# Kernel tuning notes

Measured on AMD Instinct MI355X. Metric: run time of the kernel, lower is better.

## Reference

```python
import jax, jax.numpy as jnp
import numpy as np

HEAD_DIM = 64
FEAT_DIM = 64
WINDOW = 64
EPS = 1e-6


def _performer_phi(x, proj):
    # x: [..., D] float32, proj: [F, D]  ->  [..., F]
    scaled = x / (HEAD_DIM ** 0.25)
    projected = jnp.einsum('...d,fd->...f', scaled, proj)
    sq_norm = 0.5 * jnp.sum(scaled * scaled, axis=-1, keepdims=True)
    logits = jnp.clip(projected - sq_norm, -20.0, 20.0)
    return jnp.exp(logits) / np.sqrt(float(FEAT_DIM))


def setup_inputs() -> dict:
    key = jax.random.key(0)
    kq, kk, kv, kp = jax.random.split(key, 4)
    B, H, Hkv, T, D = 2, 32, 8, 4096, HEAD_DIM
    q = jax.random.normal(kq, (B, H, T, D), dtype=jnp.float32)
    k = jax.random.normal(kk, (B, Hkv, T, D), dtype=jnp.float32)
    v = jax.random.normal(kv, (B, Hkv, T, D), dtype=jnp.float32)
    # performer projection: orthogonal block, row-normalized (as in _build_projection_matrix)
    g = np.asarray(jax.random.normal(kp, (D, D), dtype=jnp.float32))
    qm, _ = np.linalg.qr(g)
    mat = qm[:, :FEAT_DIM].T  # [F, D]
    mat = mat / np.maximum(np.linalg.norm(mat, axis=-1, keepdims=True), 1e-6)
    proj = jnp.asarray(mat, dtype=jnp.float32)
    return {'q': q, 'k': k, 'v': v, 'proj': proj}


def reference(q, k, v, proj):
    # Hybrid attention: exact local-window softmax (current + previous block,
    # causal) fused with linear (Performer) attention over all fully-evicted
    # blocks via a recurrent SSD state, sharing a single normalizer.
    B, H, T, D = q.shape
    Hkv = k.shape[1]
    G = H // Hkv  # query heads per kv group (query_to_kv = arange(H) // G)
    W = WINDOW
    nb = T // W
    f32 = jnp.float32

    phi_q = _performer_phi(q.astype(f32), proj.astype(f32))  # [B,H,T,F]
    phi_k = _performer_phi(k.astype(f32), proj.astype(f32))  # [B,Hkv,T,F]

    pq = phi_q.reshape(B, Hkv, G, nb, W, FEAT_DIM)
    pk = phi_k.reshape(B, Hkv, nb, W, FEAT_DIM)
    qb = q.astype(f32).reshape(B, Hkv, G, nb, W, D)
    kb = k.astype(f32).reshape(B, Hkv, nb, W, D)
    vb = v.astype(f32).reshape(B, Hkv, nb, W, D)

    # ---- linear-attention recurrent state (state_decay = 1.0 -> plain cumsum)
    # state at query block c covers all blocks <= c-2 (blocks fully outside the
    # local window).
    S_blk = jnp.einsum('bknwf,bknwd->bknfd', pk, vb)  # [B,Hkv,nb,F,D]
    z_blk = pk.sum(axis=3)                            # [B,Hkv,nb,F]
    S_cum = jnp.cumsum(S_blk, axis=2)
    z_cum = jnp.cumsum(z_blk, axis=2)
    S_used = jnp.concatenate([jnp.zeros_like(S_cum[:, :, :2]), S_cum[:, :, :-2]], axis=2)
    z_used = jnp.concatenate([jnp.zeros_like(z_cum[:, :, :2]), z_cum[:, :, :-2]], axis=2)

    num_lin = jnp.einsum('bkgnwf,bknfd->bkgnwd', pq, S_used)  # [B,Hkv,G,nb,W,D]
    den_lin = jnp.einsum('bkgnwf,bknf->bkgnw', pq, z_used)    # [B,Hkv,G,nb,W]

    # ---- local softmax attention over [previous block | current block]
    k_prev = jnp.concatenate([jnp.zeros_like(kb[:, :, :1]), kb[:, :, :-1]], axis=2)
    v_prev = jnp.concatenate([jnp.zeros_like(vb[:, :, :1]), vb[:, :, :-1]], axis=2)
    kk2 = jnp.concatenate([k_prev, kb], axis=3)  # [B,Hkv,nb,2W,D]
    vv2 = jnp.concatenate([v_prev, vb], axis=3)

    scores = jnp.einsum('bkgnwd,bknxd->bkgnwx', qb, kk2) / np.sqrt(float(D))
    jj = jnp.arange(W)[:, None]        # query offset in block
    ii = jnp.arange(2 * W)[None, :]    # key offset in 2-block window
    causal = ii <= (W + jj)            # [W, 2W]
    has_prev = (jnp.arange(nb) > 0)[:, None, None]
    mask = causal[None] & (has_prev | (ii >= W)[None])  # [nb, W, 2W]
    a = jnp.where(mask[None, None, None], jnp.exp(jnp.clip(scores, -30.0, 30.0)), 0.0)

    num_loc = jnp.einsum('bkgnwx,bknxd->bkgnwd', a, vv2)
    den = a.sum(axis=-1) + den_lin + EPS  # shared normalizer

    out = (num_loc + num_lin) / den[..., None]
    return out.reshape(B, H, T, D).astype(q.dtype)
```

## Files before the change

### kernel.cpp

```cpp
#include <hip/hip_runtime.h>

#define BB 2
#define HKV 8
#define HH 32
#define TT 4096
#define NBLK 64
#define SCL 0.35355339059327373f
#define LOG2E 1.4426950408889634f

typedef __attribute__((ext_vector_type(8))) short short8;
typedef __attribute__((ext_vector_type(4))) float f32x4;
typedef unsigned int u32;

__device__ __forceinline__ unsigned short f2bf(float x) {
    union { float f; u32 u; } v; v.f = x;
    u32 r = v.u + 0x7fffu + ((v.u >> 16) & 1u);
    return (unsigned short)(r >> 16);
}
__device__ __forceinline__ u32 pk2(float lo, float hi) {
    u32 r;
    asm("v_cvt_pk_bf16_f32 %0, %1, %2" : "=v"(r) : "v"(lo), "v"(hi));
    return r;
}
__device__ __forceinline__ float bf2f(unsigned short b) {
    union { u32 u; float f; } v; v.u = ((u32)b) << 16; return v.f;
}
__device__ __forceinline__ f32x4 mfma16(short8 a, short8 b, f32x4 c) {
    return __builtin_amdgcn_mfma_f32_16x16x32_bf16(a, b, c, 0, 0, 0);
}
__device__ __forceinline__ short8 ldsfrag(const char* base, int row, int off) {
    int b = (row << 7) + off;
    b ^= (row & 7) << 4;
    return *(const short8*)(base + b);
}
__device__ __forceinline__ short8 xform(f32x4 t0, f32x4 t1, int lane) {
    const int c = lane & 15, g = lane >> 4;
    u32 p00 = pk2(t0[0], t0[1]), p01 = pk2(t0[2], t0[3]);
    u32 p10 = pk2(t1[0], t1[1]), p11 = pk2(t1[2], t1[3]);
    int srcA = c + 32 * (g & 1);
    int srcB = srcA + 16;
    u32 a00 = (u32)__shfl((int)p00, srcA);
    u32 a01 = (u32)__shfl((int)p01, srcA);
    u32 a10 = (u32)__shfl((int)p10, srcA);
    u32 a11 = (u32)__shfl((int)p11, srcA);
    u32 b00 = (u32)__shfl((int)p00, srcB);
    u32 b01 = (u32)__shfl((int)p01, srcB);
    u32 b10 = (u32)__shfl((int)p10, srcB);
    u32 b11 = (u32)__shfl((int)p11, srcB);
    bool hi = (g & 2);
    union { u32 u[4]; short8 s; } r;
    r.u[0] = hi ? a10 : a00;
    r.u[1] = hi ? a11 : a01;
    r.u[2] = hi ? b10 : b00;
    r.u[3] = hi ? b11 : b01;
    return r.s;
}
__device__ __forceinline__ void gld16(const void* g, void* l) {
    __builtin_amdgcn_global_load_lds((const __attribute__((address_space(1))) u32*)g,
                                     (__attribute__((address_space(3))) u32*)l, 16, 0, 0);
}

__global__ __launch_bounds__(256, 4) void k_phase1(
        const float* __restrict__ kg, const float* __restrict__ vg,
        const float* __restrict__ pg,
        char* __restrict__ sblk, char* __restrict__ kbf, char* __restrict__ vbf,
        float* __restrict__ zg) {
    __shared__ __align__(16) char kb_s[8192];
    __shared__ __align__(16) char vt_s[8192];
    __shared__ float sqn_s[64];

    const int tid = threadIdx.x;
    const int bid = blockIdx.x;
    const size_t base = (size_t)bid * 4096;

#pragma unroll
    for (int j = 0; j < 4; ++j) {
        int i4 = tid + j * 256;
        int key = i4 >> 4, d0 = (i4 & 15) << 2;
        float4 fk = *(const float4*)(kg + base + key * 64 + d0);
        float s0 = fk.x * SCL, s1 = fk.y * SCL, s2 = fk.z * SCL, s3 = fk.w * SCL;
        int byte = (key << 7) + (d0 << 1); byte ^= (key & 7) << 4;
        *(uint2*)(kb_s + byte) = make_uint2(pk2(s0, s1), pk2(s2, s3));
        float ps = 0.5f * (s0 * s0 + s1 * s1 + s2 * s2 + s3 * s3);
        ps += __shfl_xor(ps, 1);
        ps += __shfl_xor(ps, 2);
        ps += __shfl_xor(ps, 4);
        ps += __shfl_xor(ps, 8);
        if ((tid & 15) == 0) sqn_s[key] = ps;
    }
    {
        int d = tid & 63, kq = tid >> 6;
        const float* vp = vg + base + (size_t)kq * 16 * 64 + d;
        union { unsigned short h[16]; uint4 q[2]; } pk;
#pragma unroll
        for (int i = 0; i < 16; ++i) pk.h[i] = f2bf(vp[i * 64]);
        int b0 = ((d << 7) + (kq << 5)) ^ ((d & 7) << 4);
        int b1 = ((d << 7) + (kq << 5) + 16) ^ ((d & 7) << 4);
        *(uint4*)(vt_s + b0) = pk.q[0];
        *(uint4*)(vt_s + b1) = pk.q[1];
    }
    __syncthreads();

    {
        int off = tid * 16;
        *(float4*)(kbf + (size_t)bid * 8192 + off) = *(const float4*)(kb_s + off);
        *(float4*)(kbf + (size_t)bid * 8192 + off + 4096) = *(const float4*)(kb_s + off + 4096);
        *(float4*)(vbf + (size_t)bid * 8192 + off) = *(const float4*)(vt_s + off);
        *(float4*)(vbf + (size_t)bid * 8192 + off + 4096) = *(const float4*)(vt_s + off + 4096);
    }

    const int lane = tid & 63, wv = tid >> 6;
    const int c = lane & 15, g = lane >> 4;
    const int fb = wv * 16;

    const float* prow = pg + (size_t)(fb + c) * 64;
    short8 pjb[2];
#pragma unroll
    for (int kt = 0; kt < 2; ++kt) {
        int d0 = kt * 32 + g * 8;
        float4 f0 = *(const float4*)(prow + d0);
        float4 f1 = *(const float4*)(prow + d0 + 4);
        union { u32 u[4]; short8 s; } r;
        r.u[0] = pk2(f0.x, f0.y); r.u[1] = pk2(f0.z, f0.w);
        r.u[2] = pk2(f1.x, f1.y); r.u[3] = pk2(f1.z, f1.w);
        pjb[kt] = r.s;
    }

    f32x4 pc[4];
    float zp = 0.f;
#pragma unroll
    for (int t = 0; t < 4; ++t) {
        f32x4 s = {0.f, 0.f, 0.f, 0.f};
        s = mfma16(ldsfrag(kb_s, t * 16 + c, g * 16), pjb[0], s);
        s = mfma16(ldsfrag(kb_s, t * 16 + c, g * 16 + 64), pjb[1], s);
#pragma unroll
        for (int r = 0; r < 4; ++r) {
            int w = t * 16 + g * 4 + r;
            float p = exp2f(fmaf(s[r] - sqn_s[w], LOG2E, -3.0f));
            s[r] = p;
            zp += p;
        }
        pc[t] = s;
    }
    zp += __shfl_xor(zp, 16);
    zp += __shfl_xor(zp, 32);
    if (lane < 16) zg[(size_t)bid * 64 + fb + c] = zp;

    short8 pb0 = xform(pc[0], pc[1], lane);
    short8 pb1 = xform(pc[2], pc[3], lane);

    char* so = sblk + (size_t)bid * 8192;
#pragma unroll
    for (int dt = 0; dt < 4; ++dt) {
        f32x4 s = {0.f, 0.f, 0.f, 0.f};
        s = mfma16(ldsfrag(vt_s, dt * 16 + c, g * 16), pb0, s);
        s = mfma16(ldsfrag(vt_s, dt * 16 + c, g * 16 + 64), pb1, s);
#pragma unroll
        for (int r = 0; r < 4; ++r) {
            int d = dt * 16 + g * 4 + r;
            int byte = ((d << 7) + ((fb + c) << 1)) ^ ((d & 7) << 4);
            *(unsigned short*)(so + byte) = f2bf(s[r]);
        }
    }
}

__global__ __launch_bounds__(256) void k_scan(char* __restrict__ sblk,
                                              float* __restrict__ zg,
                                              const float* __restrict__ pg,
                                              char* __restrict__ pbf) {
    const int tid = threadIdx.x;
    const int bx = blockIdx.x;
    if (bx < 128) {
        int pair = bx >> 3;
        int u = ((bx & 7) << 8) + tid;
        char* p = sblk + (size_t)pair * 64 * 8192 + (size_t)u * 4;
        float c0a = 0.f, c1a = 0.f, c0b = 0.f, c1b = 0.f;
        for (int n = 0; n < 64; ++n) {
            u32 w = *(const u32*)(p + (size_t)n * 8192);
            float va = bf2f((unsigned short)(w & 0xffff));
            float vb = bf2f((unsigned short)(w >> 16));
            *(u32*)(p + (size_t)n * 8192) = pk2(c0a, c0b);
            c0a = c1a; c1a += va;
            c0b = c1b; c1b += vb;
        }
    } else if (bx < 132) {
        int i = ((bx - 128) << 8) + tid;
        int pair = i >> 6, f = i & 63;
        float* zp = zg + (size_t)pair * 64 * 64 + f;
        float c0 = 0.f, c1 = 0.f;
        for (int n = 0; n < 64; ++n) {
            float val = zp[(size_t)n * 64];
            zp[(size_t)n * 64] = c0;
            c0 = c1; c1 += val;
        }
    } else {
#pragma unroll
        for (int j = 0; j < 4; ++j) {
            int i4 = tid + j * 256;
            int row = i4 >> 4, d0 = (i4 & 15) << 2;
            float4 f = *(const float4*)(pg + row * 64 + d0);
            int byte = ((row << 7) + (d0 << 1)) ^ ((row & 7) << 4);
            *(uint2*)(pbf + byte) = make_uint2(pk2(f.x, f.y), pk2(f.z, f.w));
        }
    }
}

__global__ __launch_bounds__(256, 4) void k_main(
        const float* __restrict__ qg,
        const char* __restrict__ kbf, const char* __restrict__ vbf,
        const char* __restrict__ sbf, const char* __restrict__ pbf,
        const float* __restrict__ zg, float* __restrict__ outg) {
    __shared__ __align__(16) char smem[24576];

    const int tid = threadIdx.x;
    const int orig = blockIdx.x;
    const int bid = (orig & 7) * 512 + (orig >> 3);
    const int n = bid & 63;
    const int h = (bid >> 6) & 31;
    const int b = bid >> 11;
    const int kv = h >> 2;
    const int iblk = ((b * HKV + kv) << 6) + n;
    const int lane = tid & 63, wv = tid >> 6;
    const int c = lane & 15, g = lane >> 4;
    const bool hasprev = (n > 0);

    const size_t qrow0 = (size_t)(b * HH + h) * TT + (size_t)n * 64;
    const int qr = wv * 16 + c;
    const float* qrow = qg + (qrow0 + qr) * 64;
    float4 qf[4];
    qf[0] = *(const float4*)(qrow + g * 8);
    qf[1] = *(const float4*)(qrow + g * 8 + 4);
    qf[2] = *(const float4*)(qrow + 32 + g * 8);
    qf[3] = *(const float4*)(qrow + 32 + g * 8 + 4);

    {
        const char* gs[3] = {kbf + (size_t)(iblk - 1) * 8192, kbf + (size_t)iblk * 8192,
                             vbf + (size_t)iblk * 8192};
#pragma unroll
        for (int ci = 0; ci < 6; ++ci) {
            int cch = wv * 6 + ci;
            int seg = cch >> 3, off = (cch & 7) << 10;
            if (n == 0 && seg == 0) continue;
            gld16(gs[seg] + off + lane * 16, smem + (seg << 13) + off);
        }
        if (n == 0) {
            uint4 zz = {0, 0, 0, 0};
            *(uint4*)(smem + tid * 32) = zz;
            *(uint4*)(smem + tid * 32 + 16) = zz;
        }
    }

    float4 zv[4];
#pragma unroll
    for (int ft = 0; ft < 4; ++ft)
        zv[ft] = *(const float4*)(zg + (size_t)iblk * 64 + ft * 16 + g * 4);

    float sq = 0.f;
    short8 qb[2];
#pragma unroll
    for (int kt = 0; kt < 2; ++kt) {
        float4 f0 = qf[kt * 2], f1 = qf[kt * 2 + 1];
        float s0 = f0.x * SCL, s1 = f0.y * SCL, s2 = f0.z * SCL, s3 = f0.w * SCL;
        float s4 = f1.x * SCL, s5 = f1.y * SCL, s6 = f1.z * SCL, s7 = f1.w * SCL;
        sq += s0 * s0 + s1 * s1 + s2 * s2 + s3 * s3 + s4 * s4 + s5 * s5 + s6 * s6 + s7 * s7;
        union { u32 u[4]; short8 s; } r;
        r.u[0] = pk2(s0, s1); r.u[1] = pk2(s2, s3);
        r.u[2] = pk2(s4, s5); r.u[3] = pk2(s6, s7);
        qb[kt] = r.s;
    }
    sq += __shfl_xor(sq, 16);
    sq += __shfl_xor(sq, 32);
    const float sqn = 0.5f * sq;

    __syncthreads();

    const char* K2 = smem;
    const char* VTP = smem;
    const char* VTC = smem + 16384;
    const char* PJ = pbf;

    short8 ab[4];
    float asum = 0.f;
#pragma unroll
    for (int p = 0; p < 4; ++p) {
        if (p == 2) {
            __syncthreads();
            if (hasprev) {
                const char* vp = vbf + (size_t)(iblk - 1) * 8192;
                gld16(vp + ((wv * 2 + 0) << 10) + lane * 16, smem + ((wv * 2 + 0) << 10));
                gld16(vp + ((wv * 2 + 1) << 10) + lane * 16, smem + ((wv * 2 + 1) << 10));
            }
        }
        f32x4 t0, t1;
#pragma unroll
        for (int half = 0; half < 2; ++half) {
            int t = p * 2 + half;
            f32x4 sc = {0.f, 0.f, 0.f, 0.f};
            sc = mfma16(ldsfrag(K2, t * 16 + c, g * 16), qb[0], sc);
            sc = mfma16(ldsfrag(K2, t * 16 + c, g * 16 + 64), qb[1], sc);
#pragma unroll
            for (int r = 0; r < 4; ++r) {
                int key = t * 16 + g * 4 + r;
                bool valid = (key >= 64) ? ((key - 64) <= qr) : hasprev;
                float a = valid ? __expf(sc[r]) : 0.f;
                sc[r] = a;
                asum += a;
            }
            if (half == 0) t0 = sc; else t1 = sc;
        }
        ab[p] = xform(t0, t1, lane);
    }
    asum += __shfl_xor(asum, 16);
    asum += __shfl_xor(asum, 32);

    float dl = 0.f;
    short8 pb[2];
#pragma unroll
    for (int pp = 0; pp < 2; ++pp) {
        f32x4 u0, u1;
#pragma unroll
        for (int half = 0; half < 2; ++half) {
            int ft = pp * 2 + half;
            f32x4 pf = {0.f, 0.f, 0.f, 0.f};
            pf = mfma16(ldsfrag(PJ, ft * 16 + c, g * 16), qb[0], pf);
            pf = mfma16(ldsfrag(PJ, ft * 16 + c, g * 16 + 64), qb[1], pf);
#pragma unroll
            for (int r = 0; r < 4; ++r) {
                float pv = exp2f(fmaf(pf[r] - sqn, LOG2E, -3.0f));
                pf[r] = pv;
                dl += pv * ((const float*)&zv[ft])[r];
            }
            if (half == 0) u0 = pf; else u1 = pf;
        }
        pb[pp] = xform(u0, u1, lane);
    }
    dl += __shfl_xor(dl, 16);
    dl += __shfl_xor(dl, 32);

    __syncthreads();

    const char* stp = sbf + (size_t)iblk * 8192;
    const float inv = 1.f / (asum + dl + 1e-6f);
    float* orow = outg + (qrow0 + qr) * 64;
#pragma unroll
    for (int dt = 0; dt < 4; ++dt) {
        f32x4 a4 = {0.f, 0.f, 0.f, 0.f};
        a4 = mfma16(ldsfrag(VTP, dt * 16 + c, g * 16), ab[0], a4);
        a4 = mfma16(ldsfrag(VTP, dt * 16 + c, g * 16 + 64), ab[1], a4);
        a4 = mfma16(ldsfrag(VTC, dt * 16 + c, g * 16), ab[2], a4);
        a4 = mfma16(ldsfrag(VTC, dt * 16 + c, g * 16 + 64), ab[3], a4);
        a4 = mfma16(ldsfrag(stp, dt * 16 + c, g * 16), pb[0], a4);
        a4 = mfma16(ldsfrag(stp, dt * 16 + c, g * 16 + 64), pb[1], a4);
#pragma unroll
        for (int r = 0; r < 4; ++r)
            orow[dt * 16 + g * 4 + r] = a4[r] * inv;
    }
}

extern "C" void kernel_launch(void* const* d_in, const int* in_sizes, int n_in,
                              void* d_out, int out_size, void* d_ws, size_t ws_size,
                              hipStream_t stream) {
    const float* q = (const float*)d_in[0];
    const float* k = (const float*)d_in[1];
    const float* v = (const float*)d_in[2];
    const float* proj = (const float*)d_in[3];
    float* out = (float*)d_out;

    char* ws = (char*)d_ws;
    char* sblk = ws;
    char* kbf = ws + (8u << 20);
    char* vbf = ws + (16u << 20);
    float* z = (float*)(ws + (24u << 20));
    char* pbf = ws + (24u << 20) + (256u << 10);

    k_phase1<<<dim3(1024), dim3(256), 0, stream>>>(k, v, proj, sblk, kbf, vbf, z);
    k_scan<<<dim3(133), dim3(256), 0, stream>>>(sblk, z, proj, pbf);
    k_main<<<dim3(4096), dim3(256), 0, stream>>>(q, kbf, vbf, sblk, pbf, z, out);
}
```

Measured before the change: 59.91 us.

## Process strips of four blocks per workgroup with triple-buffered K/V prefetch

```diff
diff --git a/kernel.cpp b/kernel.cpp
--- a/kernel.cpp
+++ b/kernel.cpp
@@ -5,6 +5,7 @@
 #define HH 32
 #define TT 4096
 #define NBLK 64
+#define STRIP 4
 #define SCL 0.35355339059327373f
 #define LOG2E 1.4426950408889634f
 
@@ -175,23 +176,34 @@
         int u = ((bx & 7) << 8) + tid;
         char* p = sblk + (size_t)pair * 64 * 8192 + (size_t)u * 4;
         float c0a = 0.f, c1a = 0.f, c0b = 0.f, c1b = 0.f;
-        for (int n = 0; n < 64; ++n) {
-            u32 w = *(const u32*)(p + (size_t)n * 8192);
-            float va = bf2f((unsigned short)(w & 0xffff));
-            float vb = bf2f((unsigned short)(w >> 16));
-            *(u32*)(p + (size_t)n * 8192) = pk2(c0a, c0b);
-            c0a = c1a; c1a += va;
-            c0b = c1b; c1b += vb;
+        for (int n8 = 0; n8 < 64; n8 += 8) {
+            u32 w[8];
+#pragma unroll
+            for (int j = 0; j < 8; ++j)
+                w[j] = *(const u32*)(p + (size_t)(n8 + j) * 8192);
+#pragma unroll
+            for (int j = 0; j < 8; ++j) {
+                *(u32*)(p + (size_t)(n8 + j) * 8192) = pk2(c0a, c0b);
+                float va = bf2f((unsigned short)(w[j] & 0xffff));
+                float vb = bf2f((unsigned short)(w[j] >> 16));
+                c0a = c1a; c1a += va;
+                c0b = c1b; c1b += vb;
+            }
         }
     } else if (bx < 132) {
         int i = ((bx - 128) << 8) + tid;
         int pair = i >> 6, f = i & 63;
         float* zp = zg + (size_t)pair * 64 * 64 + f;
         float c0 = 0.f, c1 = 0.f;
-        for (int n = 0; n < 64; ++n) {
-            float val = zp[(size_t)n * 64];
-            zp[(size_t)n * 64] = c0;
-            c0 = c1; c1 += val;
+        for (int n8 = 0; n8 < 64; n8 += 8) {
+            float w[8];
+#pragma unroll
+            for (int j = 0; j < 8; ++j) w[j] = zp[(size_t)(n8 + j) * 64];
+#pragma unroll
+            for (int j = 0; j < 8; ++j) {
+                zp[(size_t)(n8 + j) * 64] = c0;
+                c0 = c1; c1 += w[j];
+            }
         }
     } else {
 #pragma unroll
@@ -205,155 +217,194 @@
     }
 }
 
-__global__ __launch_bounds__(256, 4) void k_main(
+__global__ __launch_bounds__(256, 3) void k_main(
         const float* __restrict__ qg,
         const char* __restrict__ kbf, const char* __restrict__ vbf,
         const char* __restrict__ sbf, const char* __restrict__ pbf,
         const float* __restrict__ zg, float* __restrict__ outg) {
-    __shared__ __align__(16) char smem[24576];
+    __shared__ __align__(16) char smem[49152];
 
     const int tid = threadIdx.x;
     const int orig = blockIdx.x;
-    const int bid = (orig & 7) * 512 + (orig >> 3);
-    const int n = bid & 63;
-    const int h = (bid >> 6) & 31;
-    const int b = bid >> 11;
-    const int kv = h >> 2;
-    const int iblk = ((b * HKV + kv) << 6) + n;
+    const int bid = (orig & 7) * 128 + (orig >> 3);
+    const int gq = bid & 3;
+    const int strip = (bid >> 2) & 15;
+    const int kv = (bid >> 6) & 7;
+    const int b = (bid >> 9) & 1;
+    const int h = kv * 4 + gq;
+    const int n0 = strip * STRIP;
+    const int iblk0 = ((b * HKV + kv) << 6) + n0;
     const int lane = tid & 63, wv = tid >> 6;
     const int c = lane & 15, g = lane >> 4;
-    const bool hasprev = (n > 0);
-
-    const size_t qrow0 = (size_t)(b * HH + h) * TT + (size_t)n * 64;
     const int qr = wv * 16 + c;
-    const float* qrow = qg + (qrow0 + qr) * 64;
+
+    {
+        const char* gs[4] = {kbf + (size_t)(iblk0 - 1) * 8192, kbf + (size_t)iblk0 * 8192,
+                             vbf + (size_t)(iblk0 - 1) * 8192, vbf + (size_t)iblk0 * 8192};
+        const int ls[4] = {0, 8192, 24576, 32768};
+#pragma unroll
+        for (int ci = 0; ci < 8; ++ci) {
+            int cch = wv * 8 + ci;
+            int seg = cch >> 3, off = (cch & 7) << 10;
+            if (n0 == 0 && (seg == 0 || seg == 2)) continue;
+            gld16(gs[seg] + off + lane * 16, smem + ls[seg] + off);
+        }
+        if (n0 == 0) {
+            uint4 zz = {0, 0, 0, 0};
+            *(uint4*)(smem + 24576 + tid * 32) = zz;
+            *(uint4*)(smem + 24576 + tid * 32 + 16) = zz;
+        }
+    }
+
+    short8 pja[8];
+#pragma unroll
+    for (int ft = 0; ft < 4; ++ft) {
+        pja[ft * 2 + 0] = ldsfrag(pbf, ft * 16 + c, g * 16);
+        pja[ft * 2 + 1] = ldsfrag(pbf, ft * 16 + c, g * 16 + 64);
+    }
+
+    const size_t qhead = (size_t)(b * HH + h) * TT;
     float4 qf[4];
-    qf[0] = *(const float4*)(qrow + g * 8);
-    qf[1] = *(const float4*)(qrow + g * 8 + 4);
-    qf[2] = *(const float4*)(qrow + 32 + g * 8);
-    qf[3] = *(const float4*)(qrow + 32 + g * 8 + 4);
-
     {
-        const char* gs[3] = {kbf + (size_t)(iblk - 1) * 8192, kbf + (size_t)iblk * 8192,
-                             vbf + (size_t)iblk * 8192};
-#pragma unroll
-        for (int ci = 0; ci < 6; ++ci) {
-            int cch = wv * 6 + ci;
-            int seg = cch >> 3, off = (cch & 7) << 10;
-            if (n == 0 && seg == 0) continue;
-            gld16(gs[seg] + off + lane * 16, smem + (seg << 13) + off);
-        }
-        if (n == 0) {
-            uint4 zz = {0, 0, 0, 0};
-            *(uint4*)(smem + tid * 32) = zz;
-            *(uint4*)(smem + tid * 32 + 16) = zz;
-        }
-    }
-
+        const float* qrow = qg + (qhead + (size_t)n0 * 64 + qr) * 64;
+        qf[0] = *(const float4*)(qrow + g * 8);
+        qf[1] = *(const float4*)(qrow + g * 8 + 4);
+        qf[2] = *(const float4*)(qrow + 32 + g * 8);
+        qf[3] = *(const float4*)(qrow + 32 + g * 8 + 4);
+    }
     float4 zv[4];
 #pragma unroll
     for (int ft = 0; ft < 4; ++ft)
-        zv[ft] = *(const float4*)(zg + (size_t)iblk * 64 + ft * 16 + g * 4);
-
-    float sq = 0.f;
-    short8 qb[2];
-#pragma unroll
-    for (int kt = 0; kt < 2; ++kt) {
-        float4 f0 = qf[kt * 2], f1 = qf[kt * 2 + 1];
-        float s0 = f0.x * SCL, s1 = f0.y * SCL, s2 = f0.z * SCL, s3 = f0.w * SCL;
-        float s4 = f1.x * SCL, s5 = f1.y * SCL, s6 = f1.z * SCL, s7 = f1.w * SCL;
-        sq += s0 * s0 + s1 * s1 + s2 * s2 + s3 * s3 + s4 * s4 + s5 * s5 + s6 * s6 + s7 * s7;
-        union { u32 u[4]; short8 s; } r;
-        r.u[0] = pk2(s0, s1); r.u[1] = pk2(s2, s3);
-        r.u[2] = pk2(s4, s5); r.u[3] = pk2(s6, s7);
-        qb[kt] = r.s;
-    }
-    sq += __shfl_xor(sq, 16);
-    sq += __shfl_xor(sq, 32);
-    const float sqn = 0.5f * sq;
+        zv[ft] = *(const float4*)(zg + (size_t)iblk0 * 64 + ft * 16 + g * 4);
 
     __syncthreads();
 
-    const char* K2 = smem;
-    const char* VTP = smem;
-    const char* VTC = smem + 16384;
-    const char* PJ = pbf;
-
-    short8 ab[4];
-    float asum = 0.f;
-#pragma unroll
-    for (int p = 0; p < 4; ++p) {
-        if (p == 2) {
-            __syncthreads();
-            if (hasprev) {
-                const char* vp = vbf + (size_t)(iblk - 1) * 8192;
-                gld16(vp + ((wv * 2 + 0) << 10) + lane * 16, smem + ((wv * 2 + 0) << 10));
-                gld16(vp + ((wv * 2 + 1) << 10) + lane * 16, smem + ((wv * 2 + 1) << 10));
+#pragma unroll 1
+    for (int i = 0; i < STRIP; ++i) {
+        const int n = n0 + i;
+        const int iblk = iblk0 + i;
+        const int prv = i % 3, cur = (i + 1) % 3, nxt = (i + 2) % 3;
+        const bool hasprev = (n > 0);
+
+        {
+            int pblk = iblk + 1; if (pblk > 1023) pblk = 1023;
+            const char* kp = kbf + (size_t)pblk * 8192;
+            const char* vp = vbf + (size_t)pblk * 8192;
+#pragma unroll
+            for (int ci = 0; ci < 2; ++ci) {
+                int off = ((wv * 2 + ci) << 10);
+                gld16(kp + off + lane * 16, smem + nxt * 8192 + off);
+                gld16(vp + off + lane * 16, smem + 24576 + nxt * 8192 + off);
             }
         }
-        f32x4 t0, t1;
-#pragma unroll
-        for (int half = 0; half < 2; ++half) {
-            int t = p * 2 + half;
-            f32x4 sc = {0.f, 0.f, 0.f, 0.f};
-            sc = mfma16(ldsfrag(K2, t * 16 + c, g * 16), qb[0], sc);
-            sc = mfma16(ldsfrag(K2, t * 16 + c, g * 16 + 64), qb[1], sc);
-#pragma unroll
-            for (int r = 0; r < 4; ++r) {
-                int key = t * 16 + g * 4 + r;
-                bool valid = (key >= 64) ? ((key - 64) <= qr) : hasprev;
-                float a = valid ? __expf(sc[r]) : 0.f;
-                sc[r] = a;
-                asum += a;
+        float4 qn[4], zn[4];
+        {
+            int nn = (i < STRIP - 1) ? n + 1 : n;
+            const float* qrow = qg + (qhead + (size_t)nn * 64 + qr) * 64;
+            qn[0] = *(const float4*)(qrow + g * 8);
+            qn[1] = *(const float4*)(qrow + g * 8 + 4);
+            qn[2] = *(const float4*)(qrow + 32 + g * 8);
+            qn[3] = *(const float4*)(qrow + 32 + g * 8 + 4);
+            int zb = iblk + 1; if (zb > 1023) zb = 1023;
+#pragma unroll
+            for (int ft = 0; ft < 4; ++ft)
+                zn[ft] = *(const float4*)(zg + (size_t)zb * 64 + ft * 16 + g * 4);
+        }
+
+        float sq = 0.f;
+        short8 qb[2];
+#pragma unroll
+        for (int kt = 0; kt < 2; ++kt) {
+            float4 f0 = qf[kt * 2], f1 = qf[kt * 2 + 1];
+            float s0 = f0.x * SCL, s1 = f0.y * SCL, s2 = f0.z * SCL, s3 = f0.w * SCL;
+            float s4 = f1.x * SCL, s5 = f1.y * SCL, s6 = f1.z * SCL, s7 = f1.w * SCL;
+            sq += s0 * s0 + s1 * s1 + s2 * s2 + s3 * s3 + s4 * s4 + s5 * s5 + s6 * s6 + s7 * s7;
+            union { u32 u[4]; short8 s; } r;
+            r.u[0] = pk2(s0, s1); r.u[1] = pk2(s2, s3);
+            r.u[2] = pk2(s4, s5); r.u[3] = pk2(s6, s7);
+            qb[kt] = r.s;
+        }
+        sq += __shfl_xor(sq, 16);
+        sq += __shfl_xor(sq, 32);
+        const float sqn = 0.5f * sq;
+
+        const char* Kprv = smem + prv * 8192;
+        const char* Kcur = smem + cur * 8192;
+        const char* Vprv = smem + 24576 + prv * 8192;
+        const char* Vcur = smem + 24576 + cur * 8192;
+
+        short8 ab[4];
+        float asum = 0.f;
+#pragma unroll
+        for (int p = 0; p < 4; ++p) {
+            f32x4 t0, t1;
+#pragma unroll
+            for (int half = 0; half < 2; ++half) {
+                int t = p * 2 + half;
+                const char* kb = (t < 4) ? Kprv : Kcur;
+                int row = (t & 3) * 16 + c;
+                f32x4 sc = {0.f, 0.f, 0.f, 0.f};
+                sc = mfma16(ldsfrag(kb, row, g * 16), qb[0], sc);
+                sc = mfma16(ldsfrag(kb, row, g * 16 + 64), qb[1], sc);
+#pragma unroll
+                for (int r = 0; r < 4; ++r) {
+                    int key = t * 16 + g * 4 + r;
+                    bool valid = (key >= 64) ? ((key - 64) <= qr) : hasprev;
+                    float a = valid ? __expf(sc[r]) : 0.f;
+                    sc[r] = a;
+                    asum += a;
+                }
+                if (half == 0) t0 = sc; else t1 = sc;
             }
-            if (half == 0) t0 = sc; else t1 = sc;
-        }
-        ab[p] = xform(t0, t1, lane);
-    }
-    asum += __shfl_xor(asum, 16);
-    asum += __shfl_xor(asum, 32);
-
-    float dl = 0.f;
-    short8 pb[2];
-#pragma unroll
-    for (int pp = 0; pp < 2; ++pp) {
-        f32x4 u0, u1;
-#pragma unroll
-        for (int half = 0; half < 2; ++half) {
-            int ft = pp * 2 + half;
-            f32x4 pf = {0.f, 0.f, 0.f, 0.f};
-            pf = mfma16(ldsfrag(PJ, ft * 16 + c, g * 16), qb[0], pf);
-            pf = mfma16(ldsfrag(PJ, ft * 16 + c, g * 16 + 64), qb[1], pf);
-#pragma unroll
-            for (int r = 0; r < 4; ++r) {
-                float pv = exp2f(fmaf(pf[r] - sqn, LOG2E, -3.0f));
-                pf[r] = pv;
-                dl += pv * ((const float*)&zv[ft])[r];
+            ab[p] = xform(t0, t1, lane);
+        }
+        asum += __shfl_xor(asum, 16);
+        asum += __shfl_xor(asum, 32);
+
+        float dl = 0.f;
+        short8 pb[2];
+#pragma unroll
+        for (int pp = 0; pp < 2; ++pp) {
+            f32x4 u0, u1;
+#pragma unroll
+            for (int half = 0; half < 2; ++half) {
+                int ft = pp * 2 + half;
+                f32x4 pf = {0.f, 0.f, 0.f, 0.f};
+                pf = mfma16(pja[ft * 2 + 0], qb[0], pf);
+                pf = mfma16(pja[ft * 2 + 1], qb[1], pf);
+#pragma unroll
+                for (int r = 0; r < 4; ++r) {
+                    float pv = exp2f(fmaf(pf[r] - sqn, LOG2E, -3.0f));
+                    pf[r] = pv;
+                    dl += pv * ((const float*)&zv[ft])[r];
+                }
+                if (half == 0) u0 = pf; else u1 = pf;
             }
-            if (half == 0) u0 = pf; else u1 = pf;
-        }
-        pb[pp] = xform(u0, u1, lane);
-    }
-    dl += __shfl_xor(dl, 16);
-    dl += __shfl_xor(dl, 32);
-
-    __syncthreads();
-
-    const char* stp = sbf + (size_t)iblk * 8192;
-    const float inv = 1.f / (asum + dl + 1e-6f);
-    float* orow = outg + (qrow0 + qr) * 64;
-#pragma unroll
-    for (int dt = 0; dt < 4; ++dt) {
-        f32x4 a4 = {0.f, 0.f, 0.f, 0.f};
-        a4 = mfma16(ldsfrag(VTP, dt * 16 + c, g * 16), ab[0], a4);
-        a4 = mfma16(ldsfrag(VTP, dt * 16 + c, g * 16 + 64), ab[1], a4);
-        a4 = mfma16(ldsfrag(VTC, dt * 16 + c, g * 16), ab[2], a4);
-        a4 = mfma16(ldsfrag(VTC, dt * 16 + c, g * 16 + 64), ab[3], a4);
-        a4 = mfma16(ldsfrag(stp, dt * 16 + c, g * 16), pb[0], a4);
-        a4 = mfma16(ldsfrag(stp, dt * 16 + c, g * 16 + 64), pb[1], a4);
-#pragma unroll
-        for (int r = 0; r < 4; ++r)
-            orow[dt * 16 + g * 4 + r] = a4[r] * inv;
+            pb[pp] = xform(u0, u1, lane);
+        }
+        dl += __shfl_xor(dl, 16);
+        dl += __shfl_xor(dl, 32);
+
+        const char* stp = sbf + (size_t)iblk * 8192;
+        const float inv = 1.f / (asum + dl + 1e-6f);
+        float* orow = outg + (qhead + (size_t)n * 64 + qr) * 64;
+#pragma unroll
+        for (int dt = 0; dt < 4; ++dt) {
+            f32x4 a4 = {0.f, 0.f, 0.f, 0.f};
+            a4 = mfma16(ldsfrag(Vprv, dt * 16 + c, g * 16), ab[0], a4);
+            a4 = mfma16(ldsfrag(Vprv, dt * 16 + c, g * 16 + 64), ab[1], a4);
+            a4 = mfma16(ldsfrag(Vcur, dt * 16 + c, g * 16), ab[2], a4);
+            a4 = mfma16(ldsfrag(Vcur, dt * 16 + c, g * 16 + 64), ab[3], a4);
+            a4 = mfma16(ldsfrag(stp, dt * 16 + c, g * 16), pb[0], a4);
+            a4 = mfma16(ldsfrag(stp, dt * 16 + c, g * 16 + 64), pb[1], a4);
+#pragma unroll
+            for (int r = 0; r < 4; ++r)
+                orow[dt * 16 + g * 4 + r] = a4[r] * inv;
+        }
+
+#pragma unroll
+        for (int j = 0; j < 4; ++j) { qf[j] = qn[j]; zv[j] = zn[j]; }
+        __syncthreads();
     }
 }
 
@@ -375,5 +426,5 @@
 
     k_phase1<<<dim3(1024), dim3(256), 0, stream>>>(k, v, proj, sblk, kbf, vbf, z);
     k_scan<<<dim3(133), dim3(256), 0, stream>>>(sblk, z, proj, pbf);
-    k_main<<<dim3(4096), dim3(256), 0, stream>>>(q, kbf, vbf, sblk, pbf, z, out);
-}
+    k_main<<<dim3(1024), dim3(256), 0, stream>>>(q, kbf, vbf, sblk, pbf, z, out);
+}
```

Result: slower. 84.11 us (+40.4%).

## Process two query heads per block in k_main to reuse K/V tiles

Applied to the files above, without the earlier changes.

```diff
diff --git a/kernel.cpp b/kernel.cpp
--- a/kernel.cpp
+++ b/kernel.cpp
@@ -175,23 +175,34 @@
         int u = ((bx & 7) << 8) + tid;
         char* p = sblk + (size_t)pair * 64 * 8192 + (size_t)u * 4;
         float c0a = 0.f, c1a = 0.f, c0b = 0.f, c1b = 0.f;
-        for (int n = 0; n < 64; ++n) {
-            u32 w = *(const u32*)(p + (size_t)n * 8192);
-            float va = bf2f((unsigned short)(w & 0xffff));
-            float vb = bf2f((unsigned short)(w >> 16));
-            *(u32*)(p + (size_t)n * 8192) = pk2(c0a, c0b);
-            c0a = c1a; c1a += va;
-            c0b = c1b; c1b += vb;
+        for (int n8 = 0; n8 < 64; n8 += 8) {
+            u32 w[8];
+#pragma unroll
+            for (int j = 0; j < 8; ++j)
+                w[j] = *(const u32*)(p + (size_t)(n8 + j) * 8192);
+#pragma unroll
+            for (int j = 0; j < 8; ++j) {
+                *(u32*)(p + (size_t)(n8 + j) * 8192) = pk2(c0a, c0b);
+                float va = bf2f((unsigned short)(w[j] & 0xffff));
+                float vb = bf2f((unsigned short)(w[j] >> 16));
+                c0a = c1a; c1a += va;
+                c0b = c1b; c1b += vb;
+            }
         }
     } else if (bx < 132) {
         int i = ((bx - 128) << 8) + tid;
         int pair = i >> 6, f = i & 63;
         float* zp = zg + (size_t)pair * 64 * 64 + f;
         float c0 = 0.f, c1 = 0.f;
-        for (int n = 0; n < 64; ++n) {
-            float val = zp[(size_t)n * 64];
-            zp[(size_t)n * 64] = c0;
-            c0 = c1; c1 += val;
+        for (int n8 = 0; n8 < 64; n8 += 8) {
+            float w[8];
+#pragma unroll
+            for (int j = 0; j < 8; ++j) w[j] = zp[(size_t)(n8 + j) * 64];
+#pragma unroll
+            for (int j = 0; j < 8; ++j) {
+                zp[(size_t)(n8 + j) * 64] = c0;
+                c0 = c1; c1 += w[j];
+            }
         }
     } else {
 #pragma unroll
@@ -205,7 +216,7 @@
     }
 }
 
-__global__ __launch_bounds__(256, 4) void k_main(
+__global__ __launch_bounds__(256, 3) void k_main(
         const float* __restrict__ qg,
         const char* __restrict__ kbf, const char* __restrict__ vbf,
         const char* __restrict__ sbf, const char* __restrict__ pbf,
@@ -214,24 +225,31 @@
 
     const int tid = threadIdx.x;
     const int orig = blockIdx.x;
-    const int bid = (orig & 7) * 512 + (orig >> 3);
-    const int n = bid & 63;
-    const int h = (bid >> 6) & 31;
-    const int b = bid >> 11;
-    const int kv = h >> 2;
+    const int bid = (orig & 7) * 256 + (orig >> 3);
+    const int pr = bid & 1;
+    const int n = (bid >> 1) & 63;
+    const int kv = (bid >> 7) & 7;
+    const int b = bid >> 10;
+    const int h0 = kv * 4 + pr * 2;
     const int iblk = ((b * HKV + kv) << 6) + n;
     const int lane = tid & 63, wv = tid >> 6;
     const int c = lane & 15, g = lane >> 4;
+    const int qr = wv * 16 + c;
     const bool hasprev = (n > 0);
 
-    const size_t qrow0 = (size_t)(b * HH + h) * TT + (size_t)n * 64;
-    const int qr = wv * 16 + c;
-    const float* qrow = qg + (qrow0 + qr) * 64;
-    float4 qf[4];
-    qf[0] = *(const float4*)(qrow + g * 8);
-    qf[1] = *(const float4*)(qrow + g * 8 + 4);
-    qf[2] = *(const float4*)(qrow + 32 + g * 8);
-    qf[3] = *(const float4*)(qrow + 32 + g * 8 + 4);
+    const size_t qrow0A = (size_t)(b * HH + h0) * TT + (size_t)n * 64;
+    const size_t qrow0B = qrow0A + TT;
+    const float* qrowA = qg + (qrow0A + qr) * 64;
+    const float* qrowB = qg + (qrow0B + qr) * 64;
+    float4 qfA[4], qfB[4];
+    qfA[0] = *(const float4*)(qrowA + g * 8);
+    qfA[1] = *(const float4*)(qrowA + g * 8 + 4);
+    qfA[2] = *(const float4*)(qrowA + 32 + g * 8);
+    qfA[3] = *(const float4*)(qrowA + 32 + g * 8 + 4);
+    qfB[0] = *(const float4*)(qrowB + g * 8);
+    qfB[1] = *(const float4*)(qrowB + g * 8 + 4);
+    qfB[2] = *(const float4*)(qrowB + 32 + g * 8);
+    qfB[3] = *(const float4*)(qrowB + 32 + g * 8 + 4);
 
     {
         const char* gs[3] = {kbf + (size_t)(iblk - 1) * 8192, kbf + (size_t)iblk * 8192,
@@ -255,32 +273,45 @@
     for (int ft = 0; ft < 4; ++ft)
         zv[ft] = *(const float4*)(zg + (size_t)iblk * 64 + ft * 16 + g * 4);
 
-    float sq = 0.f;
-    short8 qb[2];
+    float sqA = 0.f, sqB = 0.f;
+    short8 qbA[2], qbB[2];
 #pragma unroll
     for (int kt = 0; kt < 2; ++kt) {
-        float4 f0 = qf[kt * 2], f1 = qf[kt * 2 + 1];
-        float s0 = f0.x * SCL, s1 = f0.y * SCL, s2 = f0.z * SCL, s3 = f0.w * SCL;
-        float s4 = f1.x * SCL, s5 = f1.y * SCL, s6 = f1.z * SCL, s7 = f1.w * SCL;
-        sq += s0 * s0 + s1 * s1 + s2 * s2 + s3 * s3 + s4 * s4 + s5 * s5 + s6 * s6 + s7 * s7;
-        union { u32 u[4]; short8 s; } r;
-        r.u[0] = pk2(s0, s1); r.u[1] = pk2(s2, s3);
-        r.u[2] = pk2(s4, s5); r.u[3] = pk2(s6, s7);
-        qb[kt] = r.s;
-    }
-    sq += __shfl_xor(sq, 16);
-    sq += __shfl_xor(sq, 32);
-    const float sqn = 0.5f * sq;
+        {
+            float4 f0 = qfA[kt * 2], f1 = qfA[kt * 2 + 1];
+            float s0 = f0.x * SCL, s1 = f0.y * SCL, s2 = f0.z * SCL, s3 = f0.w * SCL;
+            float s4 = f1.x * SCL, s5 = f1.y * SCL, s6 = f1.z * SCL, s7 = f1.w * SCL;
+            sqA += s0 * s0 + s1 * s1 + s2 * s2 + s3 * s3 + s4 * s4 + s5 * s5 + s6 * s6 + s7 * s7;
+            union { u32 u[4]; short8 s; } r;
+            r.u[0] = pk2(s0, s1); r.u[1] = pk2(s2, s3);
+            r.u[2] = pk2(s4, s5); r.u[3] = pk2(s6, s7);
+            qbA[kt] = r.s;
+        }
+        {
+            float4 f0 = qfB[kt * 2], f1 = qfB[kt * 2 + 1];
+            float s0 = f0.x * SCL, s1 = f0.y * SCL, s2 = f0.z * SCL, s3 = f0.w * SCL;
+            float s4 = f1.x * SCL, s5 = f1.y * SCL, s6 = f1.z * SCL, s7 = f1.w * SCL;
+            sqB += s0 * s0 + s1 * s1 + s2 * s2 + s3 * s3 + s4 * s4 + s5 * s5 + s6 * s6 + s7 * s7;
+            union { u32 u[4]; short8 s; } r;
+            r.u[0] = pk2(s0, s1); r.u[1] = pk2(s2, s3);
+            r.u[2] = pk2(s4, s5); r.u[3] = pk2(s6, s7);
+            qbB[kt] = r.s;
+        }
+    }
+    sqA += __shfl_xor(sqA, 16);
+    sqA += __shfl_xor(sqA, 32);
+    sqB += __shfl_xor(sqB, 16);
+    sqB += __shfl_xor(sqB, 32);
+    const float sqnA = 0.5f * sqA, sqnB = 0.5f * sqB;
 
     __syncthreads();
 
     const char* K2 = smem;
     const char* VTP = smem;
     const char* VTC = smem + 16384;
-    const char* PJ = pbf;
-
-    short8 ab[4];
-    float asum = 0.f;
+
+    short8 abA[4], abB[4];
+    float asumA = 0.f, asumB = 0.f;
 #pragma unroll
     for (int p = 0; p < 4; ++p) {
         if (p == 2) {
@@ -291,69 +322,105 @@
                 gld16(vp + ((wv * 2 + 1) << 10) + lane * 16, smem + ((wv * 2 + 1) << 10));
             }
         }
-        f32x4 t0, t1;
+        f32x4 tA0, tA1, tB0, tB1;
 #pragma unroll
         for (int half = 0; half < 2; ++half) {
             int t = p * 2 + half;
-            f32x4 sc = {0.f, 0.f, 0.f, 0.f};
-            sc = mfma16(ldsfrag(K2, t * 16 + c, g * 16), qb[0], sc);
-            sc = mfma16(ldsfrag(K2, t * 16 + c, g * 16 + 64), qb[1], sc);
+            short8 ka0 = ldsfrag(K2, t * 16 + c, g * 16);
+            short8 ka1 = ldsfrag(K2, t * 16 + c, g * 16 + 64);
+            f32x4 scA = {0.f, 0.f, 0.f, 0.f};
+            scA = mfma16(ka0, qbA[0], scA);
+            scA = mfma16(ka1, qbA[1], scA);
+            f32x4 scB = {0.f, 0.f, 0.f, 0.f};
+            scB = mfma16(ka0, qbB[0], scB);
+            scB = mfma16(ka1, qbB[1], scB);
 #pragma unroll
             for (int r = 0; r < 4; ++r) {
                 int key = t * 16 + g * 4 + r;
                 bool valid = (key >= 64) ? ((key - 64) <= qr) : hasprev;
-                float a = valid ? __expf(sc[r]) : 0.f;
-                sc[r] = a;
-                asum += a;
+                float aA = valid ? __expf(scA[r]) : 0.f;
+                float aB = valid ? __expf(scB[r]) : 0.f;
+                scA[r] = aA; asumA += aA;
+                scB[r] = aB; asumB += aB;
             }
-            if (half == 0) t0 = sc; else t1 = sc;
-        }
-        ab[p] = xform(t0, t1, lane);
-    }
-    asum += __shfl_xor(asum, 16);
-    asum += __shfl_xor(asum, 32);
-
-    float dl = 0.f;
-    short8 pb[2];
+            if (half == 0) { tA0 = scA; tB0 = scB; } else { tA1 = scA; tB1 = scB; }
+        }
+        abA[p] = xform(tA0, tA1, lane);
+        abB[p] = xform(tB0, tB1, lane);
+    }
+    asumA += __shfl_xor(asumA, 16);
+    asumA += __shfl_xor(asumA, 32);
+    asumB += __shfl_xor(asumB, 16);
+    asumB += __shfl_xor(asumB, 32);
+
+    float dlA = 0.f, dlB = 0.f;
+    short8 pbA[2], pbB[2];
 #pragma unroll
     for (int pp = 0; pp < 2; ++pp) {
-        f32x4 u0, u1;
+        f32x4 uA0, uA1, uB0, uB1;
 #pragma unroll
         for (int half = 0; half < 2; ++half) {
             int ft = pp * 2 + half;
-            f32x4 pf = {0.f, 0.f, 0.f, 0.f};
-            pf = mfma16(ldsfrag(PJ, ft * 16 + c, g * 16), qb[0], pf);
-            pf = mfma16(ldsfrag(PJ, ft * 16 + c, g * 16 + 64), qb[1], pf);
+            short8 pj0 = ldsfrag(pbf, ft * 16 + c, g * 16);
+            short8 pj1 = ldsfrag(pbf, ft * 16 + c, g * 16 + 64);
+            f32x4 pfA = {0.f, 0.f, 0.f, 0.f};
+            pfA = mfma16(pj0, qbA[0], pfA);
+            pfA = mfma16(pj1, qbA[1], pfA);
+            f32x4 pfB = {0.f, 0.f, 0.f, 0.f};
+            pfB = mfma16(pj0, qbB[0], pfB);
+            pfB = mfma16(pj1, qbB[1], pfB);
 #pragma unroll
             for (int r = 0; r < 4; ++r) {
-                float pv = exp2f(fmaf(pf[r] - sqn, LOG2E, -3.0f));
-                pf[r] = pv;
-                dl += pv * ((const float*)&zv[ft])[r];
+                float zr = ((const float*)&zv[ft])[r];
+                float pvA = exp2f(fmaf(pfA[r] - sqnA, LOG2E, -3.0f));
+                float pvB = exp2f(fmaf(pfB[r] - sqnB, LOG2E, -3.0f));
+                pfA[r] = pvA; dlA += pvA * zr;
+                pfB[r] = pvB; dlB += pvB * zr;
             }
-            if (half == 0) u0 = pf; else u1 = pf;
-        }
-        pb[pp] = xform(u0, u1, lane);
-    }
-    dl += __shfl_xor(dl, 16);
-    dl += __shfl_xor(dl, 32);
+            if (half == 0) { uA0 = pfA; uB0 = pfB; } else { uA1 = pfA; uB1 = pfB; }
+        }
+        pbA[pp] = xform(uA0, uA1, lane);
+        pbB[pp] = xform(uB0, uB1, lane);
+    }
+    dlA += __shfl_xor(dlA, 16);
+    dlA += __shfl_xor(dlA, 32);
+    dlB += __shfl_xor(dlB, 16);
+    dlB += __shfl_xor(dlB, 32);
 
     __syncthreads();
 
     const char* stp = sbf + (size_t)iblk * 8192;
-    const float inv = 1.f / (asum + dl + 1e-6f);
-    float* orow = outg + (qrow0 + qr) * 64;
+    const float invA = 1.f / (asumA + dlA + 1e-6f);
+    const float invB = 1.f / (asumB + dlB + 1e-6f);
+    float* orowA = outg + (qrow0A + qr) * 64;
+    float* orowB = outg + (qrow0B + qr) * 64;
 #pragma unroll
     for (int dt = 0; dt < 4; ++dt) {
-        f32x4 a4 = {0.f, 0.f, 0.f, 0.f};
-        a4 = mfma16(ldsfrag(VTP, dt * 16 + c, g * 16), ab[0], a4);
-        a4 = mfma16(ldsfrag(VTP, dt * 16 + c, g * 16 + 64), ab[1], a4);
-        a4 = mfma16(ldsfrag(VTC, dt * 16 + c, g * 16), ab[2], a4);
-        a4 = mfma16(ldsfrag(VTC, dt * 16 + c, g * 16 + 64), ab[3], a4);
-        a4 = mfma16(ldsfrag(stp, dt * 16 + c, g * 16), pb[0], a4);
-        a4 = mfma16(ldsfrag(stp, dt * 16 + c, g * 16 + 64), pb[1], a4);
-#pragma unroll
-        for (int r = 0; r < 4; ++r)
-            orow[dt * 16 + g * 4 + r] = a4[r] * inv;
+        short8 vp0 = ldsfrag(VTP, dt * 16 + c, g * 16);
+        short8 vp1 = ldsfrag(VTP, dt * 16 + c, g * 16 + 64);
+        short8 vc0 = ldsfrag(VTC, dt * 16 + c, g * 16);
+        short8 vc1 = ldsfrag(VTC, dt * 16 + c, g * 16 + 64);
+        short8 st0 = ldsfrag(stp, dt * 16 + c, g * 16);
+        short8 st1 = ldsfrag(stp, dt * 16 + c, g * 16 + 64);
+        f32x4 aA = {0.f, 0.f, 0.f, 0.f};
+        aA = mfma16(vp0, abA[0], aA);
+        aA = mfma16(vp1, abA[1], aA);
+        aA = mfma16(vc0, abA[2], aA);
+        aA = mfma16(vc1, abA[3], aA);
+        aA = mfma16(st0, pbA[0], aA);
+        aA = mfma16(st1, pbA[1], aA);
+        f32x4 aB = {0.f, 0.f, 0.f, 0.f};
+        aB = mfma16(vp0, abB[0], aB);
+        aB = mfma16(vp1, abB[1], aB);
+        aB = mfma16(vc0, abB[2], aB);
+        aB = mfma16(vc1, abB[3], aB);
+        aB = mfma16(st0, pbB[0], aB);
+        aB = mfma16(st1, pbB[1], aB);
+#pragma unroll
+        for (int r = 0; r < 4; ++r) {
+            orowA[dt * 16 + g * 4 + r] = aA[r] * invA;
+            orowB[dt * 16 + g * 4 + r] = aB[r] * invB;
+        }
     }
 }
 
@@ -375,5 +442,5 @@
 
     k_phase1<<<dim3(1024), dim3(256), 0, stream>>>(k, v, proj, sblk, kbf, vbf, z);
     k_scan<<<dim3(133), dim3(256), 0, stream>>>(sblk, z, proj, pbf);
-    k_main<<<dim3(4096), dim3(256), 0, stream>>>(q, kbf, vbf, sblk, pbf, z, out);
-}
+    k_main<<<dim3(2048), dim3(256), 0, stream>>>(q, kbf, vbf, sblk, pbf, z, out);
+}
```

Measured after the change: 58.61 us, median of 2. 2.2% less time.

## Read K/V fragments directly from global and batch scan-loop loads

Applied to the files above, without the earlier changes.

```diff
diff --git a/kernel.cpp b/kernel.cpp
--- a/kernel.cpp
+++ b/kernel.cpp
@@ -175,23 +175,34 @@
         int u = ((bx & 7) << 8) + tid;
         char* p = sblk + (size_t)pair * 64 * 8192 + (size_t)u * 4;
         float c0a = 0.f, c1a = 0.f, c0b = 0.f, c1b = 0.f;
-        for (int n = 0; n < 64; ++n) {
-            u32 w = *(const u32*)(p + (size_t)n * 8192);
-            float va = bf2f((unsigned short)(w & 0xffff));
-            float vb = bf2f((unsigned short)(w >> 16));
-            *(u32*)(p + (size_t)n * 8192) = pk2(c0a, c0b);
-            c0a = c1a; c1a += va;
-            c0b = c1b; c1b += vb;
+        for (int n8 = 0; n8 < 64; n8 += 8) {
+            u32 w[8];
+#pragma unroll
+            for (int j = 0; j < 8; ++j)
+                w[j] = *(const u32*)(p + (size_t)(n8 + j) * 8192);
+#pragma unroll
+            for (int j = 0; j < 8; ++j) {
+                *(u32*)(p + (size_t)(n8 + j) * 8192) = pk2(c0a, c0b);
+                float va = bf2f((unsigned short)(w[j] & 0xffff));
+                float vb = bf2f((unsigned short)(w[j] >> 16));
+                c0a = c1a; c1a += va;
+                c0b = c1b; c1b += vb;
+            }
         }
     } else if (bx < 132) {
         int i = ((bx - 128) << 8) + tid;
         int pair = i >> 6, f = i & 63;
         float* zp = zg + (size_t)pair * 64 * 64 + f;
         float c0 = 0.f, c1 = 0.f;
-        for (int n = 0; n < 64; ++n) {
-            float val = zp[(size_t)n * 64];
-            zp[(size_t)n * 64] = c0;
-            c0 = c1; c1 += val;
+        for (int n8 = 0; n8 < 64; n8 += 8) {
+            float w[8];
+#pragma unroll
+            for (int j = 0; j < 8; ++j) w[j] = zp[(size_t)(n8 + j) * 64];
+#pragma unroll
+            for (int j = 0; j < 8; ++j) {
+                zp[(size_t)(n8 + j) * 64] = c0;
+                c0 = c1; c1 += w[j];
+            }
         }
     } else {
 #pragma unroll
@@ -210,8 +221,6 @@
         const char* __restrict__ kbf, const char* __restrict__ vbf,
         const char* __restrict__ sbf, const char* __restrict__ pbf,
         const float* __restrict__ zg, float* __restrict__ outg) {
-    __shared__ __align__(16) char smem[24576];
-
     const int tid = threadIdx.x;
     const int orig = blockIdx.x;
     const int bid = (orig & 7) * 512 + (orig >> 3);
@@ -222,34 +231,22 @@
     const int iblk = ((b * HKV + kv) << 6) + n;
     const int lane = tid & 63, wv = tid >> 6;
     const int c = lane & 15, g = lane >> 4;
+    const int qr = wv * 16 + c;
     const bool hasprev = (n > 0);
 
+    const char* Kp = kbf + (size_t)(iblk - 1) * 8192;
+    const char* Kc = kbf + (size_t)iblk * 8192;
+    const char* Vp = vbf + (size_t)(iblk - 1) * 8192;
+    const char* Vc = vbf + (size_t)iblk * 8192;
+    const char* St = sbf + (size_t)iblk * 8192;
+
     const size_t qrow0 = (size_t)(b * HH + h) * TT + (size_t)n * 64;
-    const int qr = wv * 16 + c;
     const float* qrow = qg + (qrow0 + qr) * 64;
     float4 qf[4];
     qf[0] = *(const float4*)(qrow + g * 8);
     qf[1] = *(const float4*)(qrow + g * 8 + 4);
     qf[2] = *(const float4*)(qrow + 32 + g * 8);
     qf[3] = *(const float4*)(qrow + 32 + g * 8 + 4);
-
-    {
-        const char* gs[3] = {kbf + (size_t)(iblk - 1) * 8192, kbf + (size_t)iblk * 8192,
-                             vbf + (size_t)iblk * 8192};
-#pragma unroll
-        for (int ci = 0; ci < 6; ++ci) {
-            int cch = wv * 6 + ci;
-            int seg = cch >> 3, off = (cch & 7) << 10;
-            if (n == 0 && seg == 0) continue;
-            gld16(gs[seg] + off + lane * 16, smem + (seg << 13) + off);
-        }
-        if (n == 0) {
-            uint4 zz = {0, 0, 0, 0};
-            *(uint4*)(smem + tid * 32) = zz;
-            *(uint4*)(smem + tid * 32 + 16) = zz;
-        }
-    }
-
     float4 zv[4];
 #pragma unroll
     for (int ft = 0; ft < 4; ++ft)
@@ -272,32 +269,19 @@
     sq += __shfl_xor(sq, 32);
     const float sqn = 0.5f * sq;
 
-    __syncthreads();
-
-    const char* K2 = smem;
-    const char* VTP = smem;
-    const char* VTC = smem + 16384;
-    const char* PJ = pbf;
-
     short8 ab[4];
     float asum = 0.f;
 #pragma unroll
     for (int p = 0; p < 4; ++p) {
-        if (p == 2) {
-            __syncthreads();
-            if (hasprev) {
-                const char* vp = vbf + (size_t)(iblk - 1) * 8192;
-                gld16(vp + ((wv * 2 + 0) << 10) + lane * 16, smem + ((wv * 2 + 0) << 10));
-                gld16(vp + ((wv * 2 + 1) << 10) + lane * 16, smem + ((wv * 2 + 1) << 10));
-            }
-        }
         f32x4 t0, t1;
 #pragma unroll
         for (int half = 0; half < 2; ++half) {
             int t = p * 2 + half;
+            const char* kb = (t < 4) ? Kp : Kc;
+            int row = (t & 3) * 16 + c;
             f32x4 sc = {0.f, 0.f, 0.f, 0.f};
-            sc = mfma16(ldsfrag(K2, t * 16 + c, g * 16), qb[0], sc);
-            sc = mfma16(ldsfrag(K2, t * 16 + c, g * 16 + 64), qb[1], sc);
+            sc = mfma16(ldsfrag(kb, row, g * 16), qb[0], sc);
+            sc = mfma16(ldsfrag(kb, row, g * 16 + 64), qb[1], sc);
 #pragma unroll
             for (int r = 0; r < 4; ++r) {
                 int key = t * 16 + g * 4 + r;
@@ -322,8 +306,8 @@
         for (int half = 0; half < 2; ++half) {
             int ft = pp * 2 + half;
             f32x4 pf = {0.f, 0.f, 0.f, 0.f};
-            pf = mfma16(ldsfrag(PJ, ft * 16 + c, g * 16), qb[0], pf);
-            pf = mfma16(ldsfrag(PJ, ft * 16 + c, g * 16 + 64), qb[1], pf);
+            pf = mfma16(ldsfrag(pbf, ft * 16 + c, g * 16), qb[0], pf);
+            pf = mfma16(ldsfrag(pbf, ft * 16 + c, g * 16 + 64), qb[1], pf);
 #pragma unroll
             for (int r = 0; r < 4; ++r) {
                 float pv = exp2f(fmaf(pf[r] - sqn, LOG2E, -3.0f));
@@ -337,20 +321,18 @@
     dl += __shfl_xor(dl, 16);
     dl += __shfl_xor(dl, 32);
 
-    __syncthreads();
-
-    const char* stp = sbf + (size_t)iblk * 8192;
     const float inv = 1.f / (asum + dl + 1e-6f);
     float* orow = outg + (qrow0 + qr) * 64;
 #pragma unroll
     for (int dt = 0; dt < 4; ++dt) {
+        int row = dt * 16 + c;
         f32x4 a4 = {0.f, 0.f, 0.f, 0.f};
-        a4 = mfma16(ldsfrag(VTP, dt * 16 + c, g * 16), ab[0], a4);
-        a4 = mfma16(ldsfrag(VTP, dt * 16 + c, g * 16 + 64), ab[1], a4);
-        a4 = mfma16(ldsfrag(VTC, dt * 16 + c, g * 16), ab[2], a4);
-        a4 = mfma16(ldsfrag(VTC, dt * 16 + c, g * 16 + 64), ab[3], a4);
-        a4 = mfma16(ldsfrag(stp, dt * 16 + c, g * 16), pb[0], a4);
-        a4 = mfma16(ldsfrag(stp, dt * 16 + c, g * 16 + 64), pb[1], a4);
+        a4 = mfma16(ldsfrag(Vp, row, g * 16), ab[0], a4);
+        a4 = mfma16(ldsfrag(Vp, row, g * 16 + 64), ab[1], a4);
+        a4 = mfma16(ldsfrag(Vc, row, g * 16), ab[2], a4);
+        a4 = mfma16(ldsfrag(Vc, row, g * 16 + 64), ab[3], a4);
+        a4 = mfma16(ldsfrag(St, row, g * 16), pb[0], a4);
+        a4 = mfma16(ldsfrag(St, row, g * 16 + 64), pb[1], a4);
 #pragma unroll
         for (int r = 0; r < 4; ++r)
             orow[dt * 16 + g * 4 + r] = a4[r] * inv;
```

Result: slower. 77.91 us (+30.0%).
